# Optimization experiments

Hardware: AMD Instinct MI355X
Metric: run time of the kernel (lower is better)

Reference implementation:

```python
import jax, jax.numpy as jnp
import numpy as np

D_MODEL = 1024
B, T = 4, 2048
LN_EPS = 1e-5


def setup_inputs() -> dict:
    key = jax.random.key(0)
    ks = jax.random.split(key, 8)
    d = D_MODEL
    x = jax.random.normal(ks[0], (B, T, d), dtype=jnp.float32)
    # linear params (fan-in scaled)
    W_in = jax.random.normal(ks[1], (d, 4 * d), dtype=jnp.float32) / np.sqrt(d)
    b_in = jnp.zeros((4 * d,), dtype=jnp.float32)
    W_out = jax.random.normal(ks[2], (2 * d, d), dtype=jnp.float32) / np.sqrt(2 * d)
    b_out = jnp.zeros((d,), dtype=jnp.float32)
    # LRU initializer (matches the torch module's initializer())
    rng = np.random.default_rng(0)
    r_min, r_max = 0.9, 0.999
    u1 = rng.random(d)
    u2 = rng.random(d)
    nu_log = np.log(-0.5 * np.log(u1 * (r_max ** 2 - r_min ** 2) + r_min ** 2))
    theta_log = np.log(u2 * np.pi * 2)
    gamma_log = np.log(np.sqrt(1 - np.exp(-np.exp(nu_log)) ** 2))
    # LayerNorm affine params
    ln_w = jnp.ones((2 * d,), dtype=jnp.float32)
    ln_b = jnp.zeros((2 * d,), dtype=jnp.float32)
    return {
        "x": x,
        "W_in": W_in, "b_in": b_in,
        "nu_log": jnp.asarray(nu_log, dtype=jnp.float32),
        "theta_log": jnp.asarray(theta_log, dtype=jnp.float32),
        "gamma_log": jnp.asarray(gamma_log, dtype=jnp.float32),
        "ln_w": ln_w, "ln_b": ln_b,
        "W_out": W_out, "b_out": b_out,
    }


def _complex_scan(in_r, in_i, f_r, f_i):
    """h_t = f * h_{t-1} + in_t over axis=1, complex math in real/imag pairs."""
    def combine(l, r):
        a1r, a1i, b1r, b1i = l
        a2r, a2i, b2r, b2i = r
        ar = a2r * a1r - a2i * a1i
        ai = a2r * a1i + a2i * a1r
        br = a2r * b1r - a2i * b1i + b2r
        bi = a2r * b1i + a2i * b1r + b2i
        return (ar, ai, br, bi)
    fr = jnp.broadcast_to(f_r, in_r.shape)
    fi = jnp.broadcast_to(f_i, in_i.shape)
    _, _, hr, hi = jax.lax.associative_scan(combine, (fr, fi, in_r, in_i), axis=1)
    return hr, hi


def reference(x, W_in, b_in, nu_log, theta_log, gamma_log, ln_w, ln_b, W_out, b_out):
    d = x.shape[-1]
    u = x @ W_in + b_in                       # [B, T, 4d]
    v, o = u[..., :2 * d], u[..., 2 * d:]     # each [B, T, 2d]
    nu = jnp.exp(-jnp.exp(nu_log))            # [d]
    theta = jnp.exp(theta_log)
    gamma = jnpp_exp = jnp.exp(gamma_log)
    f_r = nu * jnp.cos(theta)
    f_i = nu * jnp.sin(theta)
    in_r = gamma * v[..., :d]                 # [B, T, d]
    in_i = gamma * v[..., d:]
    h_r, h_i = _complex_scan(in_r, in_i, f_r, f_i)
    y = jnp.concatenate([h_r, h_i], axis=-1) * jax.nn.silu(o)  # [B, T, 2d]
    mu = jnp.mean(y, axis=-1, keepdims=True)
    var = jnp.mean(jnp.square(y - mu), axis=-1, keepdims=True)
    y = (y - mu) * jax.lax.rsqrt(var + LN_EPS) * ln_w + ln_b
    return y @ W_out + b_out                  # [B, T, d]
```

## Files before the change

kernel.cpp:

```cpp
#include <hip/hip_runtime.h>
#include <hip/hip_bf16.h>

#define D_MODEL 1024
#define BB 4
#define TT 2048
#define ROWS (BB*TT)
#define NCHUNK 32
#define CHLEN 64

typedef __attribute__((ext_vector_type(8))) short short8;
typedef __attribute__((ext_vector_type(4))) float floatx4;

static __device__ __forceinline__ ushort f2bf(float f) {
    union { float f; unsigned u; } v; v.f = f;
    unsigned r = v.u + 0x7FFF + ((v.u >> 16) & 1);
    return (ushort)(r >> 16);
}
static __device__ __forceinline__ float bf2f(ushort b) {
    union { unsigned u; float f; } v; v.u = ((unsigned)b) << 16;
    return v.f;
}

#define GLOAD_LDS16(gp, lp)                                                 \
    __builtin_amdgcn_global_load_lds(                                       \
        (const __attribute__((address_space(1))) void*)(gp),                \
        (__attribute__((address_space(3))) void*)(lp), 16, 0, 0)

#define PREP_A 8192
#define PREP_B 4096
#define PREP_C 2048
__global__ __launch_bounds__(256) void prep_all(
    const float* __restrict__ x, ushort* __restrict__ xb,
    const float* __restrict__ W_in, ushort* __restrict__ WinT,
    const float* __restrict__ W_out, ushort* __restrict__ W1T,
    const float* __restrict__ lnw, const float* __restrict__ lnb,
    float* __restrict__ s1, float* __restrict__ c2,
    const float* __restrict__ nu_log, const float* __restrict__ theta_log,
    const float* __restrict__ gamma_log,
    float* __restrict__ fr, float* __restrict__ fi, float* __restrict__ gm) {
    __shared__ float smem[32 * 33 + 8 * 32 * 2];
    int bid = blockIdx.x, tid = threadIdx.x;
    if (bid < PREP_A) {
        int i = bid * 256 + tid;
        float4 v = ((const float4*)x)[i];
        ushort4 o;
        o.x = f2bf(v.x); o.y = f2bf(v.y); o.z = f2bf(v.z); o.w = f2bf(v.w);
        ((ushort4*)xb)[i] = o;
    } else if (bid < PREP_A + PREP_B) {
        int b2 = bid - PREP_A;
        int n0 = (b2 & 127) * 32, k0 = (b2 >> 7) * 32;
        int tx = tid & 31, ty = tid >> 5;
        float (*tile)[33] = (float (*)[33])smem;
#pragma unroll
        for (int j = 0; j < 4; ++j)
            tile[ty + j*8][tx] = W_in[(size_t)(k0 + ty + j*8) * 4096 + n0 + tx];
        __syncthreads();
#pragma unroll
        for (int j = 0; j < 4; ++j)
            WinT[(size_t)(n0 + ty + j*8) * 1024 + k0 + tx] = f2bf(tile[tx][ty + j*8]);
    } else if (bid < PREP_A + PREP_B + PREP_C) {
        int b2 = bid - PREP_A - PREP_B;
        int n0 = (b2 & 31) * 32, k0 = (b2 >> 5) * 32;
        int tx = tid & 31, ty = tid >> 5;
        float (*tile)[33] = (float (*)[33])smem;
        float* red1 = smem + 32 * 33;
        float* red2 = red1 + 8 * 32;
        float p1 = 0.f, p2 = 0.f;
#pragma unroll
        for (int j = 0; j < 4; ++j) {
            int k = k0 + ty + j * 8;
            float w = W_out[(size_t)k * 1024 + n0 + tx];
            float lw = lnw[k], lb = lnb[k];
            tile[ty + j*8][tx] = lw * w;
            p1 += lw * w; p2 += lb * w;
        }
        __syncthreads();
#pragma unroll
        for (int j = 0; j < 4; ++j)
            W1T[(size_t)(n0 + ty + j*8) * 2048 + k0 + tx] = f2bf(tile[tx][ty + j*8]);
        red1[ty * 32 + tx] = p1; red2[ty * 32 + tx] = p2;
        __syncthreads();
        if (ty == 0) {
            float a = 0.f, b = 0.f;
#pragma unroll
            for (int t = 0; t < 8; ++t) { a += red1[t * 32 + tx]; b += red2[t * 32 + tx]; }
            atomicAdd(&s1[n0 + tx], a);
            atomicAdd(&c2[n0 + tx], b);
        }
    } else {
        int c = (bid - PREP_A - PREP_B - PREP_C) * 256 + tid;
        if (c < D_MODEL) {
            float nu = expf(-expf(nu_log[c]));
            float th = expf(theta_log[c]);
            fr[c] = nu * cosf(th);
            fi[c] = nu * sinf(th);
            gm[c] = expf(gamma_log[c]);
        }
    }
}

#define P_PRE  do { __builtin_amdgcn_sched_barrier(0); __builtin_amdgcn_s_barrier();  \
                    asm volatile("s_waitcnt lgkmcnt(0)" ::: "memory");                \
                    __builtin_amdgcn_sched_barrier(0);                                \
                    __builtin_amdgcn_s_setprio(1); } while (0)
#define P_POST do { __builtin_amdgcn_s_setprio(0); __builtin_amdgcn_sched_barrier(0); \
                    __builtin_amdgcn_s_barrier();                                     \
                    __builtin_amdgcn_sched_barrier(0); } while (0)

__global__ __launch_bounds__(512) void gemm256(
    const ushort* __restrict__ A, const ushort* __restrict__ B,
    int K, const float* __restrict__ bias,
    const float* __restrict__ gamma,
    ushort* __restrict__ out_r, ushort* __restrict__ out_i,
    ushort* __restrict__ out_o) {
    __shared__ ushort LA[2][256 * 64];
    __shared__ ushort LB[2][256 * 64];
    int tid = threadIdx.x;
    int lane = tid & 63;
    int wave = tid >> 6;
    int wp = wave >> 2;
    int wq = wave & 3;
    int lr = lane & 15, q = lane >> 4;
    int swl = lr & 7;
    int rs8 = tid >> 3, ch = tid & 7;
    int sw8 = (ch ^ (rs8 & 7)) * 8;

    int gx = gridDim.x;
    int nwg = gx * gridDim.y;
    int lid = blockIdx.y * gx + blockIdx.x;
    int per = nwg >> 3;
    int sid = (lid & 7) * per + (lid >> 3);
    long m0 = (long)(sid / gx) * 256;
    long n0 = (long)(sid % gx) * 256;
    const int NT = K >> 6;

    const ushort* Abase = A + (size_t)(m0 + rs8) * K + sw8;
    const ushort* Bbase = B + (size_t)(n0 + rs8) * K + sw8;

    floatx4 acc[8][4] = {};

#define STG_A(kt, P, R) GLOAD_LDS16(Abase + (size_t)(R) * K + (kt), \
                                    &LA[P][((R) + rs8) * 64 + ch * 8])
#define STG_B(kt, P, R) GLOAD_LDS16(Bbase + (size_t)(R) * K + (kt), \
                                    &LB[P][((R) + rs8) * 64 + ch * 8])

    STG_A(0, 0, 0);    STG_A(0, 0, 64);
    STG_B(0, 0, 0);    STG_B(0, 0, 64);
    STG_B(0, 0, 128);  STG_B(0, 0, 192);
    STG_A(0, 0, 128);  STG_A(0, 0, 192);
    STG_A(64, 1, 0);   STG_A(64, 1, 64);
    STG_B(64, 1, 0);   STG_B(64, 1, 64);
    STG_B(64, 1, 128); STG_B(64, 1, 192);
    asm volatile("s_waitcnt vmcnt(6)" ::: "memory");
    __builtin_amdgcn_s_barrier();

    for (int t = 0; t < NT; ++t) {
        const int p = t & 1;
        int kt1 = (t + 1 < NT) ? (t + 1) << 6 : 0;
        int kt2 = (t + 2 < NT) ? (t + 2) << 6 : 0;
        short8 a[2][4], b0[2][2], b1[2][2];

#pragma unroll
        for (int ks = 0; ks < 2; ++ks) {
#pragma unroll
            for (int r = 0; r < 4; ++r)
                a[ks][r] = *(const short8*)&LA[p][(wp * 64 + r * 16 + lr) * 64 + ((ks * 4 + q) ^ swl) * 8];
#pragma unroll
            for (int c = 0; c < 2; ++c)
                b0[ks][c] = *(const short8*)&LB[p][(wq * 32 + c * 16 + lr) * 64 + ((ks * 4 + q) ^ swl) * 8];
        }
        STG_A(kt1, p ^ 1, 128); STG_A(kt1, p ^ 1, 192);
        P_PRE;
#pragma unroll
        for (int ks = 0; ks < 2; ++ks)
#pragma unroll
            for (int r = 0; r < 4; ++r)
#pragma unroll
                for (int c = 0; c < 2; ++c)
                    acc[r][c] = __builtin_amdgcn_mfma_f32_16x16x32_bf16(
                        a[ks][r], b0[ks][c], acc[r][c], 0, 0, 0);
        P_POST;

#pragma unroll
        for (int ks = 0; ks < 2; ++ks)
#pragma unroll
            for (int c = 0; c < 2; ++c)
                b1[ks][c] = *(const short8*)&LB[p][(128 + wq * 32 + c * 16 + lr) * 64 + ((ks * 4 + q) ^ swl) * 8];
        STG_A(kt2, p, 0); STG_A(kt2, p, 64);
        P_PRE;
#pragma unroll
        for (int ks = 0; ks < 2; ++ks)
#pragma unroll
            for (int r = 0; r < 4; ++r)
#pragma unroll
                for (int c = 0; c < 2; ++c)
                    acc[r][2 + c] = __builtin_amdgcn_mfma_f32_16x16x32_bf16(
                        a[ks][r], b1[ks][c], acc[r][2 + c], 0, 0, 0);
        P_POST;

#pragma unroll
        for (int ks = 0; ks < 2; ++ks)
#pragma unroll
            for (int r = 0; r < 4; ++r)
                a[ks][r] = *(const short8*)&LA[p][(128 + wp * 64 + r * 16 + lr) * 64 + ((ks * 4 + q) ^ swl) * 8];
        STG_B(kt2, p, 0); STG_B(kt2, p, 64);
        P_PRE;
#pragma unroll
        for (int ks = 0; ks < 2; ++ks)
#pragma unroll
            for (int r = 0; r < 4; ++r)
#pragma unroll
                for (int c = 0; c < 2; ++c)
                    acc[4 + r][c] = __builtin_amdgcn_mfma_f32_16x16x32_bf16(
                        a[ks][r], b0[ks][c], acc[4 + r][c], 0, 0, 0);
        P_POST;

        STG_B(kt2, p, 128); STG_B(kt2, p, 192);
        asm volatile("s_waitcnt vmcnt(6)" ::: "memory");
        P_PRE;
#pragma unroll
        for (int ks = 0; ks < 2; ++ks)
#pragma unroll
            for (int r = 0; r < 4; ++r)
#pragma unroll
                for (int c = 0; c < 2; ++c)
                    acc[4 + r][2 + c] = __builtin_amdgcn_mfma_f32_16x16x32_bf16(
                        a[ks][r], b1[ks][c], acc[4 + r][2 + c], 0, 0, 0);
        P_POST;
    }
    asm volatile("s_waitcnt vmcnt(0)" ::: "memory");

    int sector = (int)(n0 >> 10);
    if (sector < 2) {
        ushort* dst = sector ? out_i : out_r;
#pragma unroll
        for (int nh = 0; nh < 2; ++nh)
#pragma unroll
            for (int c = 0; c < 2; ++c) {
                int lc = (int)(n0 & 1023) + nh * 128 + wq * 32 + c * 16 + lr;
                float bv = bias[(sector << 10) + lc];
                float gv = gamma[lc];
#pragma unroll
                for (int mh = 0; mh < 2; ++mh)
#pragma unroll
                    for (int r = 0; r < 4; ++r)
#pragma unroll
                        for (int g = 0; g < 4; ++g) {
                            long row = m0 + mh * 128 + wp * 64 + r * 16 + q * 4 + g;
                            dst[row * 1024 + lc] = f2bf(gv * (acc[mh * 4 + r][nh * 2 + c][g] + bv));
                        }
            }
    } else {
        int oc0 = (int)(n0 - 2048);
#pragma unroll
        for (int nh = 0; nh < 2; ++nh)
#pragma unroll
            for (int c = 0; c < 2; ++c) {
                int oc = oc0 + nh * 128 + wq * 32 + c * 16 + lr;
                float bv = bias[2048 + oc];
#pragma unroll
                for (int mh = 0; mh < 2; ++mh)
#pragma unroll
                    for (int r = 0; r < 4; ++r)
#pragma unroll
                        for (int g = 0; g < 4; ++g) {
                            long row = m0 + mh * 128 + wp * 64 + r * 16 + q * 4 + g;
                            out_o[row * 2048 + oc] = f2bf(acc[mh * 4 + r][nh * 2 + c][g] + bv);
                        }
            }
    }
#undef STG_A
#undef STG_B
}

__global__ __launch_bounds__(256) void gemm128(
    const ushort* __restrict__ A, const ushort* __restrict__ B,
    int K, int N, const float* __restrict__ bias, float* __restrict__ outC,
    const float* __restrict__ mu, const float* __restrict__ rs,
    const float* __restrict__ s1, const float* __restrict__ c2) {
    __shared__ ushort As[128 * 64];
    __shared__ ushort Bs[128 * 64];
    int tid = threadIdx.x;
    int lane = tid & 63, wave = tid >> 6;
    int wm = (wave & 1) * 64, wn = (wave >> 1) * 64;
    int lr = lane & 15, q = lane >> 4;
    int gx = gridDim.x;
    int nwg = gx * gridDim.y;
    int lid = blockIdx.y * gx + blockIdx.x;
    int per = nwg >> 3;
    int sid = (lid & 7) * per + (lid >> 3);
    long m0 = (long)(sid / gx) * 128;
    long n0 = (long)(sid % gx) * 128;
    floatx4 acc[4][4] = {};

    int rs_ = tid >> 3;
    int pg = ((tid & 7) ^ (rs_ & 7)) * 8;
    const ushort* Ap = A + (m0 + rs_) * (long)K + pg;
    const ushort* Bp = B + (n0 + rs_) * (long)K + pg;
    int swl = lr & 7;

    for (int kt = 0; kt < K; kt += 64) {
        __syncthreads();
#pragma unroll
        for (int j = 0; j < 4; ++j) {
            GLOAD_LDS16(Ap + kt + (long)(j * 32) * K, &As[(j * 256 + tid) * 8]);
            GLOAD_LDS16(Bp + kt + (long)(j * 32) * K, &Bs[(j * 256 + tid) * 8]);
        }
        __syncthreads();
#pragma unroll
        for (int s = 0; s < 2; ++s) {
            short8 af[4], bfv[4];
            int pq = ((s * 4 + q) ^ swl) * 8;
#pragma unroll
            for (int r = 0; r < 4; ++r)
                af[r] = *(const short8*)&As[(wm + r * 16 + lr) * 64 + pq];
#pragma unroll
            for (int c = 0; c < 4; ++c)
                bfv[c] = *(const short8*)&Bs[(wn + c * 16 + lr) * 64 + pq];
#pragma unroll
            for (int r = 0; r < 4; ++r)
#pragma unroll
                for (int c = 0; c < 4; ++c)
                    acc[r][c] = __builtin_amdgcn_mfma_f32_16x16x32_bf16(
                        af[r], bfv[c], acc[r][c], 0, 0, 0);
        }
    }

#pragma unroll
    for (int r = 0; r < 4; ++r) {
#pragma unroll
        for (int c = 0; c < 4; ++c) {
            long col = n0 + wn + c * 16 + lr;
            float bc = c2[col] + bias[col];
            float s1c = s1[col];
#pragma unroll
            for (int g = 0; g < 4; ++g) {
                long row = m0 + wm + r * 16 + q * 4 + g;
                outC[row * (long)N + col] =
                    rs[row] * (acc[r][c][g] - mu[row] * s1c) + bc;
            }
        }
    }
}

__global__ __launch_bounds__(256) void scan_carries(
    const ushort* __restrict__ in_r, const ushort* __restrict__ in_i,
    float* __restrict__ carry,
    const float* __restrict__ fr_, const float* __restrict__ fi_) {
    int t = blockIdx.x * 256 + threadIdx.x;
    int cp = t & 511;
    int ck = (t >> 9) & (NCHUNK - 1);
    int b = t >> 14;
    int c0 = cp * 2;
    float f0r = fr_[c0], f0i = fi_[c0], f1r = fr_[c0 + 1], f1i = fi_[c0 + 1];
    size_t base = ((size_t)(b * TT + ck * CHLEN)) * 1024 + c0;
    float h0r = 0.f, h0i = 0.f, h1r = 0.f, h1i = 0.f;
#pragma unroll 8
    for (int j = 0; j < CHLEN; ++j) {
        uint ur = *(const uint*)(in_r + base + (size_t)j * 1024);
        uint ui = *(const uint*)(in_i + base + (size_t)j * 1024);
        float r0 = bf2f((ushort)ur), r1 = bf2f((ushort)(ur >> 16));
        float i0 = bf2f((ushort)ui), i1 = bf2f((ushort)(ui >> 16));
        float n0r = f0r * h0r - f0i * h0i + r0;
        float n0i = f0r * h0i + f0i * h0r + i0;
        float n1r = f1r * h1r - f1i * h1i + r1;
        float n1i = f1r * h1i + f1i * h1r + i1;
        h0r = n0r; h0i = n0i; h1r = n1r; h1i = n1i;
    }
    ((float4*)carry)[((size_t)b * NCHUNK + ck) * 512 + cp] =
        make_float4(h0r, h0i, h1r, h1i);
}

__global__ __launch_bounds__(256) void carry_prefix(
    float* __restrict__ carry,
    const float* __restrict__ fr_, const float* __restrict__ fi_) {
    int t = blockIdx.x * 256 + threadIdx.x;
    int cp = t & 511, b = t >> 9;
    int c0 = cp * 2;
    float a0r = fr_[c0], a0i = fi_[c0], a1r = fr_[c0 + 1], a1i = fi_[c0 + 1];
#pragma unroll
    for (int s = 0; s < 6; ++s) {
        float t0r = a0r * a0r - a0i * a0i, t0i = 2.f * a0r * a0i;
        float t1r = a1r * a1r - a1i * a1i, t1i = 2.f * a1r * a1i;
        a0r = t0r; a0i = t0i; a1r = t1r; a1i = t1i;
    }
    float4* base = (float4*)carry + (size_t)b * NCHUNK * 512 + cp;
    float C0r = 0.f, C0i = 0.f, C1r = 0.f, C1i = 0.f;
    for (int k = 0; k < NCHUNK; ++k) {
        float4 s = base[(size_t)k * 512];
        base[(size_t)k * 512] = make_float4(C0r, C0i, C1r, C1i);
        float n0r = a0r * C0r - a0i * C0i + s.x;
        float n0i = a0r * C0i + a0i * C0r + s.y;
        float n1r = a1r * C1r - a1i * C1i + s.z;
        float n1i = a1r * C1i + a1i * C1r + s.w;
        C0r = n0r; C0i = n0i; C1r = n1r; C1i = n1i;
    }
}

__global__ __launch_bounds__(256) void scan_apply(
    const ushort* __restrict__ in_r, const ushort* __restrict__ in_i,
    const float* __restrict__ carry,
    const float* __restrict__ fr_, const float* __restrict__ fi_,
    const ushort* __restrict__ o, ushort* __restrict__ yb) {
    int t = blockIdx.x * 256 + threadIdx.x;
    int cp = t & 511;
    int ck = (t >> 9) & (NCHUNK - 1);
    int b = t >> 14;
    int c0 = cp * 2;
    float f0r = fr_[c0], f0i = fi_[c0], f1r = fr_[c0 + 1], f1i = fi_[c0 + 1];
    float4 C = ((const float4*)carry)[((size_t)b * NCHUNK + ck) * 512 + cp];
    float h0r = C.x, h0i = C.y, h1r = C.z, h1i = C.w;
    size_t base = ((size_t)(b * TT + ck * CHLEN)) * 1024 + c0;
    size_t rowbase = (size_t)(b * TT + ck * CHLEN);
#pragma unroll 4
    for (int j = 0; j < CHLEN; ++j) {
        uint ur = *(const uint*)(in_r + base + (size_t)j * 1024);
        uint ui = *(const uint*)(in_i + base + (size_t)j * 1024);
        size_t ob = (rowbase + j) * 2048 + c0;
        uint uo1 = *(const uint*)(o + ob);
        uint uo2 = *(const uint*)(o + ob + 1024);
        float r0 = bf2f((ushort)ur), r1 = bf2f((ushort)(ur >> 16));
        float i0 = bf2f((ushort)ui), i1 = bf2f((ushort)(ui >> 16));
        float n0r = f0r * h0r - f0i * h0i + r0;
        float n0i = f0r * h0i + f0i * h0r + i0;
        float n1r = f1r * h1r - f1i * h1i + r1;
        float n1i = f1r * h1i + f1i * h1r + i1;
        h0r = n0r; h0i = n0i; h1r = n1r; h1i = n1i;
        float o00 = bf2f((ushort)uo1), o01 = bf2f((ushort)(uo1 >> 16));
        float o10 = bf2f((ushort)uo2), o11 = bf2f((ushort)(uo2 >> 16));
        float y00 = h0r * o00 / (1.f + __expf(-o00));
        float y01 = h1r * o01 / (1.f + __expf(-o01));
        float y10 = h0i * o10 / (1.f + __expf(-o10));
        float y11 = h1i * o11 / (1.f + __expf(-o11));
        *(uint*)(yb + ob) = (uint)f2bf(y00) | ((uint)f2bf(y01) << 16);
        *(uint*)(yb + ob + 1024) = (uint)f2bf(y10) | ((uint)f2bf(y11) << 16);
    }
}

__global__ __launch_bounds__(256) void row_stats(
    const ushort* __restrict__ yb, float* __restrict__ mu_o,
    float* __restrict__ rs_o) {
    long row = blockIdx.x;
    int tid = threadIdx.x;
    const ushort* p = yb + row * 2048 + tid * 8;
    uint4 raw = *(const uint4*)p;
    float s = 0.f, s2 = 0.f;
    unsigned w[4] = {raw.x, raw.y, raw.z, raw.w};
#pragma unroll
    for (int j = 0; j < 4; ++j) {
        float a = bf2f((ushort)(w[j] & 0xffff));
        float b = bf2f((ushort)(w[j] >> 16));
        s += a + b; s2 += a * a + b * b;
    }
#pragma unroll
    for (int off = 32; off > 0; off >>= 1) {
        s += __shfl_down(s, off, 64);
        s2 += __shfl_down(s2, off, 64);
    }
    __shared__ float red[8];
    int wv = tid >> 6;
    if ((tid & 63) == 0) { red[wv] = s; red[4 + wv] = s2; }
    __syncthreads();
    if (tid == 0) {
        s = red[0] + red[1] + red[2] + red[3];
        s2 = red[4] + red[5] + red[6] + red[7];
        float mu = s * (1.f / 2048.f);
        float var = s2 * (1.f / 2048.f) - mu * mu;
        mu_o[row] = mu;
        rs_o[row] = rsqrtf(var + 1e-5f);
    }
}


extern "C" void kernel_launch(void* const* d_in, const int* in_sizes, int n_in,
                              void* d_out, int out_size, void* d_ws, size_t ws_size,
                              hipStream_t stream) {
    const float* x         = (const float*)d_in[0];
    const float* W_in      = (const float*)d_in[1];
    const float* b_in      = (const float*)d_in[2];
    const float* nu_log    = (const float*)d_in[3];
    const float* theta_log = (const float*)d_in[4];
    const float* gamma_log = (const float*)d_in[5];
    const float* ln_w      = (const float*)d_in[6];
    const float* ln_b      = (const float*)d_in[7];
    const float* W_out     = (const float*)d_in[8];
    const float* b_out     = (const float*)d_in[9];
    float* out = (float*)d_out;

    char* ws = (char*)d_ws;
    size_t off = 0;
    auto alloc = [&](size_t bytes) {
        char* p = ws + off;
        off += (bytes + 255) & ~(size_t)255;
        return p;
    };
    ushort* xb    = (ushort*)alloc((size_t)ROWS * 1024 * 2);
    ushort* WinT  = (ushort*)alloc((size_t)4096 * 1024 * 2);
    ushort* W1T   = (ushort*)alloc((size_t)1024 * 2048 * 2);
    float*  fr    = (float*)alloc(1024 * 4);
    float*  fi    = (float*)alloc(1024 * 4);
    float*  gm    = (float*)alloc(1024 * 4);
    float*  s1c2  = (float*)alloc(2048 * 4);
    float*  s1    = s1c2;
    float*  c2    = s1c2 + 1024;
    ushort* in_r  = (ushort*)alloc((size_t)ROWS * 1024 * 2);
    ushort* in_i  = (ushort*)alloc((size_t)ROWS * 1024 * 2);
    ushort* obuf  = (ushort*)alloc((size_t)ROWS * 2048 * 2);
    float*  carry = (float*)alloc((size_t)BB * 1024 * NCHUNK * 2 * 4);
    ushort* yb    = (ushort*)alloc((size_t)ROWS * 2048 * 2);
    float*  muv   = (float*)alloc(ROWS * 4);
    float*  rsv   = (float*)alloc(ROWS * 4);

    hipMemsetAsync(s1c2, 0, 2048 * 4, stream);

    prep_all<<<PREP_A + PREP_B + PREP_C + 4, 256, 0, stream>>>(
        x, xb, W_in, WinT, W_out, W1T, ln_w, ln_b, s1, c2,
        nu_log, theta_log, gamma_log, fr, fi, gm);

    gemm256<<<dim3(4096 / 256, ROWS / 256), 512, 0, stream>>>(
        xb, WinT, 1024, b_in, gm, in_r, in_i, obuf);

    scan_carries<<<BB * 512 * NCHUNK / 256, 256, 0, stream>>>(in_r, in_i, carry, fr, fi);
    carry_prefix<<<BB * 512 / 256, 256, 0, stream>>>(carry, fr, fi);
    scan_apply<<<BB * 512 * NCHUNK / 256, 256, 0, stream>>>(
        in_r, in_i, carry, fr, fi, obuf, yb);

    row_stats<<<ROWS, 256, 0, stream>>>(yb, muv, rsv);

    gemm128<<<dim3(1024 / 128, ROWS / 128), 256, 0, stream>>>(
        yb, W1T, 2048, 1024, b_out, out, muv, rsv, s1, c2);
}
```

Before: 275.8 us.

## Pipeline output GEMM with double-buffered 128x256 tiles and shorten scan chunks

Replaces the single-buffered 128x128 output GEMM with a 512-thread, 128x256-tile kernel. It double-buffers LDS, issues async global-to-LDS loads two k-steps ahead, and splits each k-step into four MFMA phases interleaved with the staging loads. It also halves the scan chunk length (64 chunks of 32), adjusting the batch index and the chunk-power computation to match. This gives more parallelism in the scan passes and hides memory latency in the GEMM, at the cost of more LDS per block, fewer GEMM blocks, and a longer carry-prefix loop.

Result: no change. 273.8 us (-0.7%).

```diff
diff --git a/kernel.cpp b/kernel.cpp
--- a/kernel.cpp
+++ b/kernel.cpp
@@ -5,8 +5,8 @@
 #define BB 4
 #define TT 2048
 #define ROWS (BB*TT)
-#define NCHUNK 32
-#define CHLEN 64
+#define NCHUNK 64
+#define CHLEN 32
 
 typedef __attribute__((ext_vector_type(8))) short short8;
 typedef __attribute__((ext_vector_type(4))) float floatx4;
@@ -273,74 +273,146 @@
 #undef STG_B
 }
 
-__global__ __launch_bounds__(256) void gemm128(
+__global__ __launch_bounds__(512) void gemm2_8ph(
     const ushort* __restrict__ A, const ushort* __restrict__ B,
     int K, int N, const float* __restrict__ bias, float* __restrict__ outC,
     const float* __restrict__ mu, const float* __restrict__ rs,
     const float* __restrict__ s1, const float* __restrict__ c2) {
-    __shared__ ushort As[128 * 64];
-    __shared__ ushort Bs[128 * 64];
+    __shared__ ushort LA[2][128 * 64];
+    __shared__ ushort LB[2][256 * 64];
     int tid = threadIdx.x;
-    int lane = tid & 63, wave = tid >> 6;
-    int wm = (wave & 1) * 64, wn = (wave >> 1) * 64;
+    int lane = tid & 63;
+    int wave = tid >> 6;
+    int wp = wave >> 2;
+    int wq = wave & 3;
     int lr = lane & 15, q = lane >> 4;
+    int swl = lr & 7;
+    int rs8 = tid >> 3, ch = tid & 7;
+    int sw8 = (ch ^ (rs8 & 7)) * 8;
+
     int gx = gridDim.x;
     int nwg = gx * gridDim.y;
     int lid = blockIdx.y * gx + blockIdx.x;
     int per = nwg >> 3;
     int sid = (lid & 7) * per + (lid >> 3);
     long m0 = (long)(sid / gx) * 128;
-    long n0 = (long)(sid % gx) * 128;
+    long n0 = (long)(sid % gx) * 256;
+    const int NT = K >> 6;
+
+    const ushort* Abase = A + (size_t)(m0 + rs8) * K + sw8;
+    const ushort* Bbase = B + (size_t)(n0 + rs8) * K + sw8;
+
     floatx4 acc[4][4] = {};
 
-    int rs_ = tid >> 3;
-    int pg = ((tid & 7) ^ (rs_ & 7)) * 8;
-    const ushort* Ap = A + (m0 + rs_) * (long)K + pg;
-    const ushort* Bp = B + (n0 + rs_) * (long)K + pg;
-    int swl = lr & 7;
-
-    for (int kt = 0; kt < K; kt += 64) {
-        __syncthreads();
-#pragma unroll
-        for (int j = 0; j < 4; ++j) {
-            GLOAD_LDS16(Ap + kt + (long)(j * 32) * K, &As[(j * 256 + tid) * 8]);
-            GLOAD_LDS16(Bp + kt + (long)(j * 32) * K, &Bs[(j * 256 + tid) * 8]);
+#define STG2_A(kt, P, R) GLOAD_LDS16(Abase + (size_t)(R) * K + (kt), \
+                                     &LA[P][((R) + rs8) * 64 + ch * 8])
+#define STG2_B(kt, P, R) GLOAD_LDS16(Bbase + (size_t)(R) * K + (kt), \
+                                     &LB[P][((R) + rs8) * 64 + ch * 8])
+
+    STG2_A(0, 0, 0);   STG2_A(0, 0, 64);
+    STG2_B(0, 0, 0);   STG2_B(0, 0, 64);
+    STG2_B(0, 0, 128); STG2_B(0, 0, 192);
+    STG2_A(64, 1, 0);
+    STG2_B(64, 1, 0);  STG2_B(64, 1, 64);
+    asm volatile("s_waitcnt vmcnt(3)" ::: "memory");
+    __builtin_amdgcn_s_barrier();
+
+    for (int t = 0; t < NT; ++t) {
+        const int p = t & 1;
+        int kt1 = (t + 1 < NT) ? (t + 1) << 6 : 0;
+        int kt2 = (t + 2 < NT) ? (t + 2) << 6 : 0;
+        short8 a[2][2], b0[2][2], b1[2][2];
+
+#pragma unroll
+        for (int ks = 0; ks < 2; ++ks) {
+#pragma unroll
+            for (int r = 0; r < 2; ++r)
+                a[ks][r] = *(const short8*)&LA[p][(wp * 32 + r * 16 + lr) * 64 + ((ks * 4 + q) ^ swl) * 8];
+#pragma unroll
+            for (int c = 0; c < 2; ++c)
+                b0[ks][c] = *(const short8*)&LB[p][(wq * 32 + c * 16 + lr) * 64 + ((ks * 4 + q) ^ swl) * 8];
         }
-        __syncthreads();
-#pragma unroll
-        for (int s = 0; s < 2; ++s) {
-            short8 af[4], bfv[4];
-            int pq = ((s * 4 + q) ^ swl) * 8;
-#pragma unroll
-            for (int r = 0; r < 4; ++r)
-                af[r] = *(const short8*)&As[(wm + r * 16 + lr) * 64 + pq];
-#pragma unroll
-            for (int c = 0; c < 4; ++c)
-                bfv[c] = *(const short8*)&Bs[(wn + c * 16 + lr) * 64 + pq];
-#pragma unroll
-            for (int r = 0; r < 4; ++r)
-#pragma unroll
-                for (int c = 0; c < 4; ++c)
+        STG2_A(kt1, p ^ 1, 64);
+        STG2_B(kt1, p ^ 1, 128); STG2_B(kt1, p ^ 1, 192);
+        P_PRE;
+#pragma unroll
+        for (int ks = 0; ks < 2; ++ks)
+#pragma unroll
+            for (int r = 0; r < 2; ++r)
+#pragma unroll
+                for (int c = 0; c < 2; ++c)
                     acc[r][c] = __builtin_amdgcn_mfma_f32_16x16x32_bf16(
-                        af[r], bfv[c], acc[r][c], 0, 0, 0);
-        }
-    }
-
-#pragma unroll
-    for (int r = 0; r < 4; ++r) {
-#pragma unroll
-        for (int c = 0; c < 4; ++c) {
-            long col = n0 + wn + c * 16 + lr;
+                        a[ks][r], b0[ks][c], acc[r][c], 0, 0, 0);
+        P_POST;
+
+#pragma unroll
+        for (int ks = 0; ks < 2; ++ks)
+#pragma unroll
+            for (int c = 0; c < 2; ++c)
+                b1[ks][c] = *(const short8*)&LB[p][(128 + wq * 32 + c * 16 + lr) * 64 + ((ks * 4 + q) ^ swl) * 8];
+        P_PRE;
+#pragma unroll
+        for (int ks = 0; ks < 2; ++ks)
+#pragma unroll
+            for (int r = 0; r < 2; ++r)
+#pragma unroll
+                for (int c = 0; c < 2; ++c)
+                    acc[r][2 + c] = __builtin_amdgcn_mfma_f32_16x16x32_bf16(
+                        a[ks][r], b1[ks][c], acc[r][2 + c], 0, 0, 0);
+        P_POST;
+
+#pragma unroll
+        for (int ks = 0; ks < 2; ++ks)
+#pragma unroll
+            for (int r = 0; r < 2; ++r)
+                a[ks][r] = *(const short8*)&LA[p][(64 + wp * 32 + r * 16 + lr) * 64 + ((ks * 4 + q) ^ swl) * 8];
+        STG2_A(kt2, p, 0);
+        P_PRE;
+#pragma unroll
+        for (int ks = 0; ks < 2; ++ks)
+#pragma unroll
+            for (int r = 0; r < 2; ++r)
+#pragma unroll
+                for (int c = 0; c < 2; ++c)
+                    acc[2 + r][c] = __builtin_amdgcn_mfma_f32_16x16x32_bf16(
+                        a[ks][r], b0[ks][c], acc[2 + r][c], 0, 0, 0);
+        P_POST;
+
+        STG2_B(kt2, p, 0); STG2_B(kt2, p, 64);
+        asm volatile("s_waitcnt vmcnt(3)" ::: "memory");
+        P_PRE;
+#pragma unroll
+        for (int ks = 0; ks < 2; ++ks)
+#pragma unroll
+            for (int r = 0; r < 2; ++r)
+#pragma unroll
+                for (int c = 0; c < 2; ++c)
+                    acc[2 + r][2 + c] = __builtin_amdgcn_mfma_f32_16x16x32_bf16(
+                        a[ks][r], b1[ks][c], acc[2 + r][2 + c], 0, 0, 0);
+        P_POST;
+    }
+    asm volatile("s_waitcnt vmcnt(0)" ::: "memory");
+
+#pragma unroll
+    for (int nh = 0; nh < 2; ++nh)
+#pragma unroll
+        for (int c = 0; c < 2; ++c) {
+            long col = n0 + nh * 128 + wq * 32 + c * 16 + lr;
             float bc = c2[col] + bias[col];
             float s1c = s1[col];
 #pragma unroll
-            for (int g = 0; g < 4; ++g) {
-                long row = m0 + wm + r * 16 + q * 4 + g;
-                outC[row * (long)N + col] =
-                    rs[row] * (acc[r][c][g] - mu[row] * s1c) + bc;
-            }
+            for (int mh = 0; mh < 2; ++mh)
+#pragma unroll
+                for (int r = 0; r < 2; ++r)
+#pragma unroll
+                    for (int g = 0; g < 4; ++g) {
+                        long row = m0 + mh * 64 + wp * 32 + r * 16 + q * 4 + g;
+                        outC[row * (long)N + col] =
+                            rs[row] * (acc[mh * 2 + r][nh * 2 + c][g] - mu[row] * s1c) + bc;
+                    }
         }
-    }
+#undef STG2_A
+#undef STG2_B
 }
 
 __global__ __launch_bounds__(256) void scan_carries(
@@ -350,7 +422,7 @@
     int t = blockIdx.x * 256 + threadIdx.x;
     int cp = t & 511;
     int ck = (t >> 9) & (NCHUNK - 1);
-    int b = t >> 14;
+    int b = t >> 15;
     int c0 = cp * 2;
     float f0r = fr_[c0], f0i = fi_[c0], f1r = fr_[c0 + 1], f1i = fi_[c0 + 1];
     size_t base = ((size_t)(b * TT + ck * CHLEN)) * 1024 + c0;
@@ -379,7 +451,7 @@
     int c0 = cp * 2;
     float a0r = fr_[c0], a0i = fi_[c0], a1r = fr_[c0 + 1], a1i = fi_[c0 + 1];
 #pragma unroll
-    for (int s = 0; s < 6; ++s) {
+    for (int s = 0; s < 5; ++s) {
         float t0r = a0r * a0r - a0i * a0i, t0i = 2.f * a0r * a0i;
         float t1r = a1r * a1r - a1i * a1i, t1i = 2.f * a1r * a1i;
         a0r = t0r; a0i = t0i; a1r = t1r; a1i = t1i;
@@ -405,7 +477,7 @@
     int t = blockIdx.x * 256 + threadIdx.x;
     int cp = t & 511;
     int ck = (t >> 9) & (NCHUNK - 1);
-    int b = t >> 14;
+    int b = t >> 15;
     int c0 = cp * 2;
     float f0r = fr_[c0], f0i = fi_[c0], f1r = fr_[c0 + 1], f1i = fi_[c0 + 1];
     float4 C = ((const float4*)carry)[((size_t)b * NCHUNK + ck) * 512 + cp];
@@ -527,6 +599,6 @@
 
     row_stats<<<ROWS, 256, 0, stream>>>(yb, muv, rsv);
 
-    gemm128<<<dim3(1024 / 128, ROWS / 128), 256, 0, stream>>>(
+    gemm2_8ph<<<dim3(1024 / 256, ROWS / 128), 512, 0, stream>>>(
         yb, W1T, 2048, 1024, b_out, out, muv, rsv, s1, c2);
 }
```
